# Performance work log

Hardware: AMD Instinct MI355X
Metric: run time of the kernel (lower is better)

The kernel has to match this reference:

```python
import jax, jax.numpy as jnp
import numpy as np

B, S, D, H = 4, 2048, 1024, 16
HD = D // H  # 64

def setup_inputs() -> dict:
    key = jax.random.key(0)
    ks = jax.random.split(key, 6)
    scale = 1.0 / np.sqrt(D)
    return {
        "x": jax.random.normal(ks[0], (B, S, D), dtype=jnp.float32),
        "Wq": jax.random.normal(ks[1], (D, D), dtype=jnp.float32) * scale,
        "Wk": jax.random.normal(ks[2], (D, D), dtype=jnp.float32) * scale,
        "Wv": jax.random.normal(ks[3], (D, D), dtype=jnp.float32) * scale,
        "Wo": jax.random.normal(ks[4], (D, D), dtype=jnp.float32) * scale,
        "bo": jnp.zeros((D,), dtype=jnp.float32),
    }

def reference(x, Wq, Wk, Wv, Wo, bo):
    b, s, d = x.shape
    # projections (no bias for q/k/v, matching QKV_BIAS=False)
    q = (x @ Wq).reshape(b, s, H, HD).transpose(0, 2, 1, 3)  # [b,h,s,hd]
    k = (x @ Wk).reshape(b, s, H, HD).transpose(0, 2, 1, 3)
    v = (x @ Wv).reshape(b, s, H, HD).transpose(0, 2, 1, 3)
    scores = jnp.einsum('bhqd,bhkd->bhqk', q, k)  # [b,h,s,s]
    causal = jnp.tril(jnp.ones((s, s), dtype=bool))  # True where allowed
    scores = jnp.where(causal, scores, -jnp.inf)
    attn = jax.nn.softmax(scores / np.sqrt(HD), axis=-1)
    ctx = jnp.einsum('bhqk,bhkd->bhqd', attn, v)  # [b,h,s,hd]
    ctx = ctx.transpose(0, 2, 1, 3).reshape(b, s, d)
    return ctx @ Wo + bo
```

## Files before the change

### kernel.cpp

```cpp
#include <hip/hip_runtime.h>

#define BSZ 4
#define SEQ 2048
#define DIM 1024
#define NH  16
#define HD  64
#define QT  128
#define KT  64
#define PAD 72

typedef float v4f __attribute__((ext_vector_type(4)));
typedef short s8v __attribute__((ext_vector_type(8)));
typedef unsigned short u16;
typedef unsigned short u16x8 __attribute__((ext_vector_type(8)));
typedef unsigned short u16x4 __attribute__((ext_vector_type(4)));
typedef unsigned int u32;
typedef unsigned int u32x2 __attribute__((ext_vector_type(2)));
typedef unsigned int u32x4 __attribute__((ext_vector_type(4)));

__device__ __forceinline__ u16 f2bf(float f) {
  u32 u = __builtin_bit_cast(u32, f);
  u32 r = u + 0x7fffu + ((u >> 16) & 1u);
  return (u16)(r >> 16);
}
__device__ __forceinline__ u32 cvtpk(float lo, float hi) {
  u32 r; asm("v_cvt_pk_bf16_f32 %0, %1, %2" : "=v"(r) : "v"(lo), "v"(hi)); return r;
}
__device__ __forceinline__ u16 f2bf1(float f) { return (u16)cvtpk(f, f); }
__device__ __forceinline__ float fast_exp2(float x) {
#if __has_builtin(__builtin_amdgcn_exp2f)
  return __builtin_amdgcn_exp2f(x);
#else
  return exp2f(x);
#endif
}
__device__ __forceinline__ void gll16(const u16* g, u16* l) {
  __builtin_amdgcn_global_load_lds((const __attribute__((address_space(1))) void*)g,
                                   (__attribute__((address_space(3))) void*)l, 16, 0, 0);
}
__device__ __forceinline__ void wg_barrier() { asm volatile("s_barrier" ::: "memory"); }
#define WAITCNT_LGKM0 0xC07F
#define VMW6 __builtin_amdgcn_s_waitcnt(0xF76);
#define VMW0 __builtin_amdgcn_s_waitcnt(0xF70);

__global__ __launch_bounds__(256) void prep_kernel(const float* __restrict__ x,
                                                   u16* __restrict__ Xb,
                                                   const float* __restrict__ W0,
                                                   const float* __restrict__ W1,
                                                   const float* __restrict__ W2,
                                                   const float* __restrict__ W3,
                                                   u16* __restrict__ Wt, int n4) {
  __shared__ float tile[32][33];
  const int bid = blockIdx.x;
  if (bid < 8192) {
    int i = bid * 256 + threadIdx.x;
    if (i >= n4) return;
    v4f v = reinterpret_cast<const v4f*>(x)[i];
    u16x4 r;
    #pragma unroll
    for (int c = 0; c < 4; c++) r[c] = f2bf(v[c]);
    reinterpret_cast<u16x4*>(Xb)[i] = r;
    return;
  }
  const int b2 = bid - 8192;
  const int z = b2 >> 10, rem = b2 & 1023;
  const float* W = z == 0 ? W0 : z == 1 ? W1 : z == 2 ? W2 : W3;
  const float scale = (z == 0) ? 0.18033688011112042f : 1.0f;
  u16* T = Wt + (size_t)z * DIM * DIM;
  int tx = threadIdx.x & 31, ty = threadIdx.x >> 5;
  int bn = (rem & 31) * 32, bk = (rem >> 5) * 32;
  #pragma unroll
  for (int r = 0; r < 4; r++) {
    int k = bk + ty + r * 8;
    tile[ty + r * 8][tx] = W[(size_t)k * DIM + bn + tx];
  }
  __syncthreads();
  #pragma unroll
  for (int r = 0; r < 4; r++) {
    int n = bn + ty + r * 8;
    T[(size_t)n * DIM + bk + tx] = f2bf(tile[tx][ty + r * 8] * scale);
  }
}


#define ST_TILE(t_, s_)                                                           \
  gll16(Ag0 + (t_) * 64,      AW0 + (s_) * 16384);                                \
  gll16(Ag1 + (t_) * 64,      AW1 + (s_) * 16384);                                \
  gll16(Ag0 + (t_) * 64 + 32, AW0 + (s_) * 16384 + 8192);                         \
  gll16(Ag1 + (t_) * 64 + 32, AW1 + (s_) * 16384 + 8192);                         \
  gll16(Bg0 + (t_) * 64,      BW0 + (s_) * 8192);                                 \
  gll16(Bg0 + (t_) * 64 + 32, BW0 + (s_) * 8192 + 4096);

#define PH(t_, s_, STAGES, VMW)                                                   \
  { const u16* Ab = AL + (s_) * 16384 + aRd;                                      \
    const u16* Bb = BL + (s_) * 8192 + bRd;                                       \
    s8v af[2][4], bf[2][4];                                                       \
    _Pragma("unroll") for (int kc_ = 0; kc_ < 2; kc_++) {                         \
      _Pragma("unroll") for (int i_ = 0; i_ < 4; i_++)                            \
        af[kc_][i_] = *(const s8v*)(Ab + kc_ * 8192 + i_ * 512);                  \
      _Pragma("unroll") for (int j_ = 0; j_ < 4; j_++)                            \
        bf[kc_][j_] = *(const s8v*)(Bb + kc_ * 4096 + j_ * 512);                  \
    }                                                                             \
    STAGES                                                                        \
    VMW                                                                           \
    wg_barrier();                                                                 \
    __builtin_amdgcn_s_waitcnt(WAITCNT_LGKM0);                                    \
    __builtin_amdgcn_s_setprio(1);                                                \
    _Pragma("unroll") for (int kc_ = 0; kc_ < 2; kc_++)                           \
      _Pragma("unroll") for (int i_ = 0; i_ < 4; i_++)                            \
        _Pragma("unroll") for (int j_ = 0; j_ < 4; j_++)                          \
          acc[i_][j_] = __builtin_amdgcn_mfma_f32_16x16x32_bf16(                  \
              af[kc_][i_], bf[kc_][j_], acc[i_][j_], 0, 0, 0);                    \
    __builtin_amdgcn_s_setprio(0);                                                \
    wg_barrier(); }

#define GEMM256x128_CORE()                                                        \
  extern __shared__ __align__(16) u16 lds[];                                      \
  const int t = threadIdx.x;                                                      \
  const int lane = t & 63, w = t >> 6;                                            \
  const int waveM = w >> 1, waveN = w & 1;                                        \
  const int quad = lane >> 4, l16 = lane & 15;                                    \
  const int sR = lane & 15, sC = lane >> 4;                                       \
  u16* AL = lds;                                                                  \
  u16* BL = lds + 49152;                                                          \
  v4f acc[4][4];                                                                  \
  _Pragma("unroll") for (int i = 0; i < 4; i++)                                   \
    _Pragma("unroll") for (int j = 0; j < 4; j++)                                 \
      acc[i][j] = (v4f){0.f, 0.f, 0.f, 0.f};                                      \
  const u16* Ag0 = A + (size_t)(m0 + w * 32 + sR) * DIM + sC * 8;                 \
  const u16* Ag1 = Ag0 + 16 * DIM;                                                \
  const u16* Bg0 = Bt + (size_t)(n0 + w * 16 + sR) * DIM + sC * 8;                \
  u16* AW0 = AL + w * 1024;                                                       \
  u16* AW1 = AL + w * 1024 + 512;                                                 \
  u16* BW0 = BL + w * 512;                                                        \
  const int aRd = waveM * 2048 + quad * 128 + l16 * 8;                            \
  const int bRd = waveN * 2048 + quad * 128 + l16 * 8;                            \
  ST_TILE(0, 0) ST_TILE(1, 1)                                                     \
  VMW6                                                                            \
  wg_barrier();                                                                   \
  _Pragma("unroll") for (int t3 = 0; t3 < 12; t3 += 3) {                          \
    PH(t3 + 0, 0, ST_TILE(t3 + 2, 2), VMW6)                                       \
    PH(t3 + 1, 1, ST_TILE(t3 + 3, 0), VMW6)                                       \
    PH(t3 + 2, 2, ST_TILE(t3 + 4, 1), VMW6)                                       \
  }                                                                               \
  PH(12, 0, ST_TILE(14, 2), VMW6)                                                 \
  PH(13, 1, ST_TILE(15, 0), VMW6)                                                 \
  PH(14, 2, , VMW0)                                                               \
  PH(15, 0, , )

__global__ __launch_bounds__(512, 2) void gemm_qkv(const u16* __restrict__ A, const u16* __restrict__ Wt,
                                                   u16* __restrict__ Qb, u16* __restrict__ Kb,
                                                   u16* __restrict__ Vtg) {
  const int bid = blockIdx.x;
  const int swz = (bid & 7) * 96 + (bid >> 3);
  const int z = swz >> 8;
  const int rem = swz & 255;
  const int m0 = (rem >> 3) * 256;
  const int n0 = (rem & 7) * 128;
  const u16* Bt = Wt + (size_t)z * DIM * DIM;
  GEMM256x128_CORE()
  if (z == 2) {
    #pragma unroll
    for (int mi = 0; mi < 4; mi++) {
      #pragma unroll
      for (int ni = 0; ni < 4; ni++) {
        int gm0 = m0 + waveM * 64 + mi * 16 + quad * 4;
        int gn = n0 + waveN * 64 + ni * 16 + l16;
        int b = gm0 >> 11, s0 = gm0 & (SEQ - 1), hh = gn >> 6, d = gn & (HD - 1);
        u32x2 pw;
        pw[0] = cvtpk(acc[mi][ni][0], acc[mi][ni][1]);
        pw[1] = cvtpk(acc[mi][ni][2], acc[mi][ni][3]);
        *(u16x4*)(Vtg + ((size_t)(b * NH + hh) * HD + d) * SEQ + s0) =
            __builtin_bit_cast(u16x4, pw);
      }
    }
  } else {
    u16* C = (z == 0) ? Qb : Kb;
    #pragma unroll
    for (int mi = 0; mi < 4; mi++) {
      #pragma unroll
      for (int ni = 0; ni < 4; ni++) {
        int gn = n0 + waveN * 64 + ni * 16 + l16;
        #pragma unroll
        for (int r = 0; r < 4; r++) {
          int gm = m0 + waveM * 64 + mi * 16 + quad * 4 + r;
          C[(size_t)gm * DIM + gn] = f2bf1(acc[mi][ni][r]);
        }
      }
    }
  }
}

__global__ __launch_bounds__(512, 2) void gemm_proj(const u16* __restrict__ A, const u16* __restrict__ Bt,
                                                    float* __restrict__ Cf, const float* __restrict__ bias) {
  const int bid = blockIdx.x;
  const int swz = (bid & 7) * 32 + (bid >> 3);
  const int m0 = (swz >> 3) * 256;
  const int n0 = (swz & 7) * 128;
  GEMM256x128_CORE()
  #pragma unroll
  for (int ni = 0; ni < 4; ni++) {
    int gn = n0 + waveN * 64 + ni * 16 + l16;
    float bv = bias[gn];
    #pragma unroll
    for (int mi = 0; mi < 4; mi++) {
      #pragma unroll
      for (int r = 0; r < 4; r++) {
        int gm = m0 + waveM * 64 + mi * 16 + quad * 4 + r;
        Cf[(size_t)gm * DIM + gn] = acc[mi][ni][r] + bv;
      }
    }
  }
}

__global__ __launch_bounds__(256, 4) void flash_attn_mfma(const u16* __restrict__ Qb,
                                                          const u16* __restrict__ Kb,
                                                          const u16* __restrict__ Vtg,
                                                          u16* __restrict__ Ob) {
  const int h = blockIdx.x, px = blockIdx.y, bb = blockIdx.z;
  const int t = threadIdx.x;
  const int lane = t & 63, w = t >> 6;
  const int quad = lane >> 4, l16 = lane & 15;

  __shared__ u16 SH[QT * PAD];
  u16* const Ks = SH;
  u16* const Vs = SH + KT * PAD;

  const size_t qkbase = (size_t)bb * SEQ * DIM + h * HD;
  const size_t vbase = ((size_t)bb * NH + h) * (size_t)HD * SEQ;

  const int vrow = t >> 2, scol = (t & 3) * 16;
  const int krow = ((vrow >> 5) + 2 * ((vrow >> 2) & 1)) * 16 + ((vrow >> 3) & 3) * 4 + (vrow & 3);

  for (int pass = 0; pass < 2; pass++) {
    const int qi = (pass == 0) ? px : (SEQ / QT - 1 - px);
    const int q0 = qi * QT;
    const int wq = q0 + w * 32;
    const int ntiles = 2 * qi + 2;

    __syncthreads();

    {
      const int r = t >> 1, c0 = (t & 1) * 32;
      const u16* src = Qb + qkbase + (size_t)(q0 + r) * DIM + c0;
      #pragma unroll
      for (int ch = 0; ch < 4; ch++)
        *(u16x8*)(SH + r * PAD + c0 + ch * 8) = *(const u16x8*)(src + ch * 8);
    }
    __syncthreads();

    s8v qf[2][2];
    #pragma unroll
    for (int ni = 0; ni < 2; ni++)
      #pragma unroll
      for (int kc = 0; kc < 2; kc++)
        qf[ni][kc] = *(const s8v*)(SH + (w * 32 + ni * 16 + l16) * PAD + kc * 32 + quad * 8);

    u16x8 kr0, kr1, vr0, vr1;
    {
      const u16* kp = Kb + qkbase + (size_t)vrow * DIM + scol;
      kr0 = *(const u16x8*)kp; kr1 = *(const u16x8*)(kp + 8);
      const u16* vp = Vtg + vbase + (size_t)vrow * SEQ + scol;
      vr0 = *(const u16x8*)vp; vr1 = *(const u16x8*)(vp + 8);
    }

    float mrun[2] = {-1e30f, -1e30f}, lrun[2] = {0.f, 0.f};
    v4f O[4][2];
    #pragma unroll
    for (int di = 0; di < 4; di++)
      #pragma unroll
      for (int ni = 0; ni < 2; ni++) O[di][ni] = (v4f){0.f, 0.f, 0.f, 0.f};

    for (int it = 0; it < ntiles; ++it) {
      const int kv0 = it * KT;
      __syncthreads();
      *(u16x8*)(Ks + krow * PAD + scol) = kr0;
      *(u16x8*)(Ks + krow * PAD + scol + 8) = kr1;
      *(u16x8*)(Vs + vrow * PAD + scol) = vr0;
      *(u16x8*)(Vs + vrow * PAD + scol + 8) = vr1;
      __syncthreads();
      if (it + 1 < ntiles) {
        const int nkv = kv0 + KT;
        const u16* kp = Kb + qkbase + (size_t)(nkv + vrow) * DIM + scol;
        kr0 = *(const u16x8*)kp; kr1 = *(const u16x8*)(kp + 8);
        const u16* vp = Vtg + vbase + (size_t)vrow * SEQ + nkv + scol;
        vr0 = *(const u16x8*)vp; vr1 = *(const u16x8*)(vp + 8);
      }
      if (kv0 > wq + 31) continue;

      v4f sc[4][2];
      #pragma unroll
      for (int mi = 0; mi < 4; mi++)
        #pragma unroll
        for (int ni = 0; ni < 2; ni++) sc[mi][ni] = (v4f){0.f, 0.f, 0.f, 0.f};
      __builtin_amdgcn_s_setprio(1);
      #pragma unroll
      for (int kc = 0; kc < 2; kc++) {
        #pragma unroll
        for (int mi = 0; mi < 4; mi++) {
          s8v kf = *(const s8v*)(Ks + (mi * 16 + l16) * PAD + kc * 32 + quad * 8);
          sc[mi][0] = __builtin_amdgcn_mfma_f32_16x16x32_bf16(kf, qf[0][kc], sc[mi][0], 0, 0, 0);
          sc[mi][1] = __builtin_amdgcn_mfma_f32_16x16x32_bf16(kf, qf[1][kc], sc[mi][1], 0, 0, 0);
        }
      }
      __builtin_amdgcn_s_setprio(0);

      if (kv0 + KT > wq) {
        #pragma unroll
        for (int mi = 0; mi < 4; mi++) {
          const int kvb = kv0 + (mi & 1) * 32 + quad * 8 + (mi >> 1) * 4;
          #pragma unroll
          for (int ni = 0; ni < 2; ni++) {
            const int qg = wq + ni * 16 + l16;
            #pragma unroll
            for (int r = 0; r < 4; r++)
              if (kvb + r > qg) sc[mi][ni][r] = -1e30f;
          }
        }
      }

      float mx[2];
      #pragma unroll
      for (int ni = 0; ni < 2; ni++) {
        float m = -1e30f;
        #pragma unroll
        for (int mi = 0; mi < 4; mi++)
          #pragma unroll
          for (int r = 0; r < 4; r++) m = fmaxf(m, sc[mi][ni][r]);
        m = fmaxf(m, __shfl_xor(m, 16, 64));
        m = fmaxf(m, __shfl_xor(m, 32, 64));
        mx[ni] = m;
      }
      const bool defer = __all((mx[0] <= mrun[0] + 8.f) && (mx[1] <= mrun[1] + 8.f));
      if (!defer) {
        float alpha[2];
        #pragma unroll
        for (int ni = 0; ni < 2; ni++) {
          const float mnew = fmaxf(mrun[ni], mx[ni]);
          alpha[ni] = fast_exp2(mrun[ni] - mnew);
          mrun[ni] = mnew;
          lrun[ni] *= alpha[ni];
        }
        #pragma unroll
        for (int di = 0; di < 4; di++)
          #pragma unroll
          for (int ni = 0; ni < 2; ni++)
            #pragma unroll
            for (int r = 0; r < 4; r++) O[di][ni][r] *= alpha[ni];
      }
      #pragma unroll
      for (int ni = 0; ni < 2; ni++) {
        float rsum = 0.f;
        #pragma unroll
        for (int mi = 0; mi < 4; mi++)
          #pragma unroll
          for (int r = 0; r < 4; r++) {
            float p = fast_exp2(sc[mi][ni][r] - mrun[ni]);
            sc[mi][ni][r] = p;
            rsum += p;
          }
        rsum += __shfl_xor(rsum, 16, 64);
        rsum += __shfl_xor(rsum, 32, 64);
        lrun[ni] += rsum;
      }

      s8v pf[2][2];
      #pragma unroll
      for (int ni = 0; ni < 2; ni++)
        #pragma unroll
        for (int kc = 0; kc < 2; kc++) {
          u32x4 wds;
          wds[0] = cvtpk(sc[kc][ni][0], sc[kc][ni][1]);
          wds[1] = cvtpk(sc[kc][ni][2], sc[kc][ni][3]);
          wds[2] = cvtpk(sc[kc + 2][ni][0], sc[kc + 2][ni][1]);
          wds[3] = cvtpk(sc[kc + 2][ni][2], sc[kc + 2][ni][3]);
          pf[ni][kc] = __builtin_bit_cast(s8v, wds);
        }

      __builtin_amdgcn_s_setprio(1);
      #pragma unroll
      for (int kc = 0; kc < 2; kc++) {
        #pragma unroll
        for (int di = 0; di < 4; di++) {
          s8v vf = *(const s8v*)(Vs + (di * 16 + l16) * PAD + kc * 32 + quad * 8);
          O[di][0] = __builtin_amdgcn_mfma_f32_16x16x32_bf16(vf, pf[0][kc], O[di][0], 0, 0, 0);
          O[di][1] = __builtin_amdgcn_mfma_f32_16x16x32_bf16(vf, pf[1][kc], O[di][1], 0, 0, 0);
        }
      }
      __builtin_amdgcn_s_setprio(0);
    }

    __syncthreads();
    const float inv0 = 1.f / lrun[0], inv1 = 1.f / lrun[1];
    #pragma unroll
    for (int di = 0; di < 4; di++)
      #pragma unroll
      for (int ni = 0; ni < 2; ni++) {
        const float inv = ni ? inv1 : inv0;
        #pragma unroll
        for (int r = 0; r < 4; r++)
          SH[(w * 32 + ni * 16 + l16) * PAD + di * 16 + quad * 4 + r] = f2bf1(O[di][ni][r] * inv);
      }
    __syncthreads();
    {
      const int r = t >> 1, c0 = (t & 1) * 32;
      u16* dst = Ob + qkbase + (size_t)(q0 + r) * DIM + c0;
      #pragma unroll
      for (int ch = 0; ch < 4; ch++)
        *(u16x8*)(dst + ch * 8) = *(const u16x8*)(SH + r * PAD + c0 + ch * 8);
    }
  }
}

extern "C" void kernel_launch(void* const* d_in, const int* in_sizes, int n_in,
                              void* d_out, int out_size, void* d_ws, size_t ws_size,
                              hipStream_t stream) {
  (void)in_sizes; (void)n_in; (void)out_size; (void)ws_size;
  const float* x  = (const float*)d_in[0];
  const float* Wq = (const float*)d_in[1];
  const float* Wk = (const float*)d_in[2];
  const float* Wv = (const float*)d_in[3];
  const float* Wo = (const float*)d_in[4];
  const float* bo = (const float*)d_in[5];
  float* out = (float*)d_out;

  static bool lds_attr_done = false;
  if (!lds_attr_done) {
    hipFuncSetAttribute(reinterpret_cast<const void*>(gemm_qkv),
                        hipFuncAttributeMaxDynamicSharedMemorySize, 147456);
    hipFuncSetAttribute(reinterpret_cast<const void*>(gemm_proj),
                        hipFuncAttributeMaxDynamicSharedMemorySize, 147456);
    lds_attr_done = true;
  }

  char* ws = (char*)d_ws;
  const size_t MB = 1024ull * 1024ull;
  u16* Xb  = (u16*)(ws);
  u16* Wt  = (u16*)(ws + 16 * MB);
  u16* Qb  = (u16*)(ws + 24 * MB);
  u16* Kb  = (u16*)(ws + 40 * MB);
  u16* Vtg = (u16*)(ws + 56 * MB);
  u16* Cb  = (u16*)(ws + 72 * MB);

  const int NTOK = BSZ * SEQ;
  const int n4 = NTOK * DIM / 4;
  prep_kernel<<<dim3(12288), 256, 0, stream>>>(x, Xb, Wq, Wk, Wv, Wo, Wt, n4);

  gemm_qkv<<<dim3(768), 512, 147456, stream>>>(Xb, Wt, Qb, Kb, Vtg);

  flash_attn_mfma<<<dim3(NH, SEQ / QT / 2, BSZ), 256, 0, stream>>>(Qb, Kb, Vtg, Cb);

  gemm_proj<<<dim3(256), 512, 147456, stream>>>(Cb, Wt + 3ull * DIM * DIM, out, bo);
}
```

Measured before the change: 286.5 us.

## Enlarge attention query tile to 256 rows with one tile per block

The flash attention kernel now processes a 256-row query tile per block, with each wave owning 64 query rows instead of 32. This doubles the reuse of every K/V tile staged in LDS. The old two-pass pairing of light and heavy causal tiles is replaced by a flat 512-block grid whose index ordering interleaves short and long tiles. The trade-off is roughly double the accumulator and score registers per wave, launch bounds dropping from 4 to 2 blocks per SM, and fewer, coarser blocks that can leave the causal load unbalanced.

```diff
diff --git a/kernel.cpp b/kernel.cpp
--- a/kernel.cpp
+++ b/kernel.cpp
@@ -5,7 +5,7 @@
 #define DIM 1024
 #define NH  16
 #define HD  64
-#define QT  128
+#define QT2 256
 #define KT  64
 #define PAD 72
 
@@ -213,18 +213,20 @@
   }
 }
 
-__global__ __launch_bounds__(256, 4) void flash_attn_mfma(const u16* __restrict__ Qb,
+__global__ __launch_bounds__(256, 2) void flash_attn_mfma(const u16* __restrict__ Qb,
                                                           const u16* __restrict__ Kb,
                                                           const u16* __restrict__ Vtg,
                                                           u16* __restrict__ Ob) {
-  const int h = blockIdx.x, px = blockIdx.y, bb = blockIdx.z;
+  const int bid = blockIdx.x;
+  const int h = bid & 15, bb = (bid >> 4) & 3, u = bid >> 6;
+  const int qi = (u < 4) ? u : (11 - u);
   const int t = threadIdx.x;
   const int lane = t & 63, w = t >> 6;
   const int quad = lane >> 4, l16 = lane & 15;
 
-  __shared__ u16 SH[QT * PAD];
-  u16* const Ks = SH;
-  u16* const Vs = SH + KT * PAD;
+  __shared__ u16 QPs[QT2 * PAD];
+  __shared__ u16 Ks[KT * PAD];
+  __shared__ u16 Vs[HD * PAD];
 
   const size_t qkbase = (size_t)bb * SEQ * DIM + h * HD;
   const size_t vbase = ((size_t)bb * NH + h) * (size_t)HD * SEQ;
@@ -232,183 +234,179 @@
   const int vrow = t >> 2, scol = (t & 3) * 16;
   const int krow = ((vrow >> 5) + 2 * ((vrow >> 2) & 1)) * 16 + ((vrow >> 3) & 3) * 4 + (vrow & 3);
 
-  for (int pass = 0; pass < 2; pass++) {
-    const int qi = (pass == 0) ? px : (SEQ / QT - 1 - px);
-    const int q0 = qi * QT;
-    const int wq = q0 + w * 32;
-    const int ntiles = 2 * qi + 2;
-
+  const int q0 = qi * QT2;
+  const int wq = q0 + w * 64;
+  const int ntiles = 4 * (qi + 1);
+
+  {
+    const u16* src = Qb + qkbase + (size_t)(q0 + t) * DIM;
+    #pragma unroll
+    for (int ch = 0; ch < 8; ch++)
+      *(u16x8*)(QPs + t * PAD + ch * 8) = *(const u16x8*)(src + ch * 8);
+  }
+  __syncthreads();
+
+  s8v qf[4][2];
+  #pragma unroll
+  for (int ni = 0; ni < 4; ni++)
+    #pragma unroll
+    for (int kc = 0; kc < 2; kc++)
+      qf[ni][kc] = *(const s8v*)(QPs + (w * 64 + ni * 16 + l16) * PAD + kc * 32 + quad * 8);
+
+  u16x8 kr0, kr1, vr0, vr1;
+  {
+    const u16* kp = Kb + qkbase + (size_t)vrow * DIM + scol;
+    kr0 = *(const u16x8*)kp; kr1 = *(const u16x8*)(kp + 8);
+    const u16* vp = Vtg + vbase + (size_t)vrow * SEQ + scol;
+    vr0 = *(const u16x8*)vp; vr1 = *(const u16x8*)(vp + 8);
+  }
+
+  float mrun[4] = {-1e30f, -1e30f, -1e30f, -1e30f}, lrun[4] = {0.f, 0.f, 0.f, 0.f};
+  v4f O[4][4];
+  #pragma unroll
+  for (int di = 0; di < 4; di++)
+    #pragma unroll
+    for (int ni = 0; ni < 4; ni++) O[di][ni] = (v4f){0.f, 0.f, 0.f, 0.f};
+
+  for (int it = 0; it < ntiles; ++it) {
+    const int kv0 = it * KT;
     __syncthreads();
-
-    {
-      const int r = t >> 1, c0 = (t & 1) * 32;
-      const u16* src = Qb + qkbase + (size_t)(q0 + r) * DIM + c0;
-      #pragma unroll
-      for (int ch = 0; ch < 4; ch++)
-        *(u16x8*)(SH + r * PAD + c0 + ch * 8) = *(const u16x8*)(src + ch * 8);
-    }
+    *(u16x8*)(Ks + krow * PAD + scol) = kr0;
+    *(u16x8*)(Ks + krow * PAD + scol + 8) = kr1;
+    *(u16x8*)(Vs + vrow * PAD + scol) = vr0;
+    *(u16x8*)(Vs + vrow * PAD + scol + 8) = vr1;
     __syncthreads();
-
-    s8v qf[2][2];
-    #pragma unroll
-    for (int ni = 0; ni < 2; ni++)
-      #pragma unroll
-      for (int kc = 0; kc < 2; kc++)
-        qf[ni][kc] = *(const s8v*)(SH + (w * 32 + ni * 16 + l16) * PAD + kc * 32 + quad * 8);
-
-    u16x8 kr0, kr1, vr0, vr1;
-    {
-      const u16* kp = Kb + qkbase + (size_t)vrow * DIM + scol;
+    if (it + 1 < ntiles) {
+      const int nkv = kv0 + KT;
+      const u16* kp = Kb + qkbase + (size_t)(nkv + vrow) * DIM + scol;
       kr0 = *(const u16x8*)kp; kr1 = *(const u16x8*)(kp + 8);
-      const u16* vp = Vtg + vbase + (size_t)vrow * SEQ + scol;
+      const u16* vp = Vtg + vbase + (size_t)vrow * SEQ + nkv + scol;
       vr0 = *(const u16x8*)vp; vr1 = *(const u16x8*)(vp + 8);
     }
-
-    float mrun[2] = {-1e30f, -1e30f}, lrun[2] = {0.f, 0.f};
-    v4f O[4][2];
-    #pragma unroll
-    for (int di = 0; di < 4; di++)
-      #pragma unroll
-      for (int ni = 0; ni < 2; ni++) O[di][ni] = (v4f){0.f, 0.f, 0.f, 0.f};
-
-    for (int it = 0; it < ntiles; ++it) {
-      const int kv0 = it * KT;
-      __syncthreads();
-      *(u16x8*)(Ks + krow * PAD + scol) = kr0;
-      *(u16x8*)(Ks + krow * PAD + scol + 8) = kr1;
-      *(u16x8*)(Vs + vrow * PAD + scol) = vr0;
-      *(u16x8*)(Vs + vrow * PAD + scol + 8) = vr1;
-      __syncthreads();
-      if (it + 1 < ntiles) {
-        const int nkv = kv0 + KT;
-        const u16* kp = Kb + qkbase + (size_t)(nkv + vrow) * DIM + scol;
-        kr0 = *(const u16x8*)kp; kr1 = *(const u16x8*)(kp + 8);
-        const u16* vp = Vtg + vbase + (size_t)vrow * SEQ + nkv + scol;
-        vr0 = *(const u16x8*)vp; vr1 = *(const u16x8*)(vp + 8);
-      }
-      if (kv0 > wq + 31) continue;
-
-      v4f sc[4][2];
+    if (kv0 > wq + 63) continue;
+
+    v4f sc[4][4];
+    #pragma unroll
+    for (int mi = 0; mi < 4; mi++)
+      #pragma unroll
+      for (int ni = 0; ni < 4; ni++) sc[mi][ni] = (v4f){0.f, 0.f, 0.f, 0.f};
+    __builtin_amdgcn_s_setprio(1);
+    #pragma unroll
+    for (int kc = 0; kc < 2; kc++) {
+      #pragma unroll
+      for (int mi = 0; mi < 4; mi++) {
+        s8v kf = *(const s8v*)(Ks + (mi * 16 + l16) * PAD + kc * 32 + quad * 8);
+        #pragma unroll
+        for (int ni = 0; ni < 4; ni++)
+          sc[mi][ni] = __builtin_amdgcn_mfma_f32_16x16x32_bf16(kf, qf[ni][kc], sc[mi][ni], 0, 0, 0);
+      }
+    }
+    __builtin_amdgcn_s_setprio(0);
+
+    if (kv0 + KT > wq) {
+      #pragma unroll
+      for (int mi = 0; mi < 4; mi++) {
+        const int kvb = kv0 + (mi & 1) * 32 + quad * 8 + (mi >> 1) * 4;
+        #pragma unroll
+        for (int ni = 0; ni < 4; ni++) {
+          const int qg = wq + ni * 16 + l16;
+          #pragma unroll
+          for (int r = 0; r < 4; r++)
+            if (kvb + r > qg) sc[mi][ni][r] = -1e30f;
+        }
+      }
+    }
+
+    float mx[4];
+    #pragma unroll
+    for (int ni = 0; ni < 4; ni++) {
+      float m = -1e30f;
       #pragma unroll
       for (int mi = 0; mi < 4; mi++)
         #pragma unroll
-        for (int ni = 0; ni < 2; ni++) sc[mi][ni] = (v4f){0.f, 0.f, 0.f, 0.f};
-      __builtin_amdgcn_s_setprio(1);
+        for (int r = 0; r < 4; r++) m = fmaxf(m, sc[mi][ni][r]);
+      m = fmaxf(m, __shfl_xor(m, 16, 64));
+      m = fmaxf(m, __shfl_xor(m, 32, 64));
+      mx[ni] = m;
+    }
+    const bool defer = __all((mx[0] <= mrun[0] + 8.f) && (mx[1] <= mrun[1] + 8.f) &&
+                             (mx[2] <= mrun[2] + 8.f) && (mx[3] <= mrun[3] + 8.f));
+    if (!defer) {
+      float alpha[4];
+      #pragma unroll
+      for (int ni = 0; ni < 4; ni++) {
+        const float mnew = fmaxf(mrun[ni], mx[ni]);
+        alpha[ni] = fast_exp2(mrun[ni] - mnew);
+        mrun[ni] = mnew;
+        lrun[ni] *= alpha[ni];
+      }
+      #pragma unroll
+      for (int di = 0; di < 4; di++)
+        #pragma unroll
+        for (int ni = 0; ni < 4; ni++)
+          #pragma unroll
+          for (int r = 0; r < 4; r++) O[di][ni][r] *= alpha[ni];
+    }
+    #pragma unroll
+    for (int ni = 0; ni < 4; ni++) {
+      float rsum = 0.f;
+      #pragma unroll
+      for (int mi = 0; mi < 4; mi++)
+        #pragma unroll
+        for (int r = 0; r < 4; r++) {
+          float p = fast_exp2(sc[mi][ni][r] - mrun[ni]);
+          sc[mi][ni][r] = p;
+          rsum += p;
+        }
+      rsum += __shfl_xor(rsum, 16, 64);
+      rsum += __shfl_xor(rsum, 32, 64);
+      lrun[ni] += rsum;
+    }
+
+    s8v pf[4][2];
+    #pragma unroll
+    for (int ni = 0; ni < 4; ni++)
       #pragma unroll
       for (int kc = 0; kc < 2; kc++) {
-        #pragma unroll
-        for (int mi = 0; mi < 4; mi++) {
-          s8v kf = *(const s8v*)(Ks + (mi * 16 + l16) * PAD + kc * 32 + quad * 8);
-          sc[mi][0] = __builtin_amdgcn_mfma_f32_16x16x32_bf16(kf, qf[0][kc], sc[mi][0], 0, 0, 0);
-          sc[mi][1] = __builtin_amdgcn_mfma_f32_16x16x32_bf16(kf, qf[1][kc], sc[mi][1], 0, 0, 0);
-        }
-      }
-      __builtin_amdgcn_s_setprio(0);
-
-      if (kv0 + KT > wq) {
-        #pragma unroll
-        for (int mi = 0; mi < 4; mi++) {
-          const int kvb = kv0 + (mi & 1) * 32 + quad * 8 + (mi >> 1) * 4;
-          #pragma unroll
-          for (int ni = 0; ni < 2; ni++) {
-            const int qg = wq + ni * 16 + l16;
-            #pragma unroll
-            for (int r = 0; r < 4; r++)
-              if (kvb + r > qg) sc[mi][ni][r] = -1e30f;
-          }
-        }
-      }
-
-      float mx[2];
-      #pragma unroll
-      for (int ni = 0; ni < 2; ni++) {
-        float m = -1e30f;
-        #pragma unroll
-        for (int mi = 0; mi < 4; mi++)
-          #pragma unroll
-          for (int r = 0; r < 4; r++) m = fmaxf(m, sc[mi][ni][r]);
-        m = fmaxf(m, __shfl_xor(m, 16, 64));
-        m = fmaxf(m, __shfl_xor(m, 32, 64));
-        mx[ni] = m;
-      }
-      const bool defer = __all((mx[0] <= mrun[0] + 8.f) && (mx[1] <= mrun[1] + 8.f));
-      if (!defer) {
-        float alpha[2];
-        #pragma unroll
-        for (int ni = 0; ni < 2; ni++) {
-          const float mnew = fmaxf(mrun[ni], mx[ni]);
-          alpha[ni] = fast_exp2(mrun[ni] - mnew);
-          mrun[ni] = mnew;
-          lrun[ni] *= alpha[ni];
-        }
-        #pragma unroll
-        for (int di = 0; di < 4; di++)
-          #pragma unroll
-          for (int ni = 0; ni < 2; ni++)
-            #pragma unroll
-            for (int r = 0; r < 4; r++) O[di][ni][r] *= alpha[ni];
-      }
-      #pragma unroll
-      for (int ni = 0; ni < 2; ni++) {
-        float rsum = 0.f;
-        #pragma unroll
-        for (int mi = 0; mi < 4; mi++)
-          #pragma unroll
-          for (int r = 0; r < 4; r++) {
-            float p = fast_exp2(sc[mi][ni][r] - mrun[ni]);
-            sc[mi][ni][r] = p;
-            rsum += p;
-          }
-        rsum += __shfl_xor(rsum, 16, 64);
-        rsum += __shfl_xor(rsum, 32, 64);
-        lrun[ni] += rsum;
-      }
-
-      s8v pf[2][2];
-      #pragma unroll
-      for (int ni = 0; ni < 2; ni++)
-        #pragma unroll
-        for (int kc = 0; kc < 2; kc++) {
-          u32x4 wds;
-          wds[0] = cvtpk(sc[kc][ni][0], sc[kc][ni][1]);
-          wds[1] = cvtpk(sc[kc][ni][2], sc[kc][ni][3]);
-          wds[2] = cvtpk(sc[kc + 2][ni][0], sc[kc + 2][ni][1]);
-          wds[3] = cvtpk(sc[kc + 2][ni][2], sc[kc + 2][ni][3]);
-          pf[ni][kc] = __builtin_bit_cast(s8v, wds);
-        }
-
-      __builtin_amdgcn_s_setprio(1);
-      #pragma unroll
-      for (int kc = 0; kc < 2; kc++) {
-        #pragma unroll
-        for (int di = 0; di < 4; di++) {
-          s8v vf = *(const s8v*)(Vs + (di * 16 + l16) * PAD + kc * 32 + quad * 8);
-          O[di][0] = __builtin_amdgcn_mfma_f32_16x16x32_bf16(vf, pf[0][kc], O[di][0], 0, 0, 0);
-          O[di][1] = __builtin_amdgcn_mfma_f32_16x16x32_bf16(vf, pf[1][kc], O[di][1], 0, 0, 0);
-        }
-      }
-      __builtin_amdgcn_s_setprio(0);
-    }
-
-    __syncthreads();
-    const float inv0 = 1.f / lrun[0], inv1 = 1.f / lrun[1];
-    #pragma unroll
-    for (int di = 0; di < 4; di++)
-      #pragma unroll
-      for (int ni = 0; ni < 2; ni++) {
-        const float inv = ni ? inv1 : inv0;
-        #pragma unroll
-        for (int r = 0; r < 4; r++)
-          SH[(w * 32 + ni * 16 + l16) * PAD + di * 16 + quad * 4 + r] = f2bf1(O[di][ni][r] * inv);
-      }
-    __syncthreads();
-    {
-      const int r = t >> 1, c0 = (t & 1) * 32;
-      u16* dst = Ob + qkbase + (size_t)(q0 + r) * DIM + c0;
-      #pragma unroll
-      for (int ch = 0; ch < 4; ch++)
-        *(u16x8*)(dst + ch * 8) = *(const u16x8*)(SH + r * PAD + c0 + ch * 8);
-    }
+        u32x4 wds;
+        wds[0] = cvtpk(sc[kc][ni][0], sc[kc][ni][1]);
+        wds[1] = cvtpk(sc[kc][ni][2], sc[kc][ni][3]);
+        wds[2] = cvtpk(sc[kc + 2][ni][0], sc[kc + 2][ni][1]);
+        wds[3] = cvtpk(sc[kc + 2][ni][2], sc[kc + 2][ni][3]);
+        pf[ni][kc] = __builtin_bit_cast(s8v, wds);
+      }
+
+    __builtin_amdgcn_s_setprio(1);
+    #pragma unroll
+    for (int kc = 0; kc < 2; kc++) {
+      #pragma unroll
+      for (int di = 0; di < 4; di++) {
+        s8v vf = *(const s8v*)(Vs + (di * 16 + l16) * PAD + kc * 32 + quad * 8);
+        #pragma unroll
+        for (int ni = 0; ni < 4; ni++)
+          O[di][ni] = __builtin_amdgcn_mfma_f32_16x16x32_bf16(vf, pf[ni][kc], O[di][ni], 0, 0, 0);
+      }
+    }
+    __builtin_amdgcn_s_setprio(0);
+  }
+
+  float inv[4];
+  #pragma unroll
+  for (int ni = 0; ni < 4; ni++) inv[ni] = 1.f / lrun[ni];
+  #pragma unroll
+  for (int di = 0; di < 4; di++)
+    #pragma unroll
+    for (int ni = 0; ni < 4; ni++) {
+      #pragma unroll
+      for (int r = 0; r < 4; r++)
+        QPs[(w * 64 + ni * 16 + l16) * PAD + di * 16 + quad * 4 + r] = f2bf1(O[di][ni][r] * inv[ni]);
+    }
+  __syncthreads();
+  {
+    u16* dst = Ob + qkbase + (size_t)(q0 + t) * DIM;
+    #pragma unroll
+    for (int ch = 0; ch < 8; ch++)
+      *(u16x8*)(dst + ch * 8) = *(const u16x8*)(QPs + t * PAD + ch * 8);
   }
 }
 
@@ -448,7 +446,7 @@
 
   gemm_qkv<<<dim3(768), 512, 147456, stream>>>(Xb, Wt, Qb, Kb, Vtg);
 
-  flash_attn_mfma<<<dim3(NH, SEQ / QT / 2, BSZ), 256, 0, stream>>>(Qb, Kb, Vtg, Cb);
+  flash_attn_mfma<<<dim3(512), 256, 0, stream>>>(Qb, Kb, Vtg, Cb);
 
   gemm_proj<<<dim3(256), 512, 147456, stream>>>(Cb, Wt + 3ull * DIM * DIM, out, bo);
 }
```

After: 275.9 us. 3.7% less time.
